# Kernel optimization log

Measured on AMD Instinct MI355X. Metric: run time of the kernel, lower is better.

Reference implementation:

```python
import jax, jax.numpy as jnp
import numpy as np

B, H = 32, 1024  # seq_len == hidden_size (required by the original code's shapes)
S = H

def setup_inputs() -> dict:
    key = jax.random.key(0)
    k1, k2, k3, k4, k5 = jax.random.split(key, 5)
    hidden = jax.random.normal(k1, (B, H), dtype=jnp.float32)
    encoder_outputs = jax.random.normal(k2, (B, S, H), dtype=jnp.float32)
    # nn.Linear(2H -> H): weight [H, 2H], bias [H]
    lim = 1.0 / np.sqrt(2 * H)
    W = jax.random.uniform(k3, (H, 2 * H), dtype=jnp.float32, minval=-lim, maxval=lim)
    b = jax.random.uniform(k4, (H,), dtype=jnp.float32, minval=-lim, maxval=lim)
    # v ~ Normal(0, 1/H)
    v = jax.random.normal(k5, (H,), dtype=jnp.float32) * (1.0 / H)
    return {"hidden": hidden, "encoder_outputs": encoder_outputs, "W": W, "b": b, "v": v}

def reference(hidden, encoder_outputs, W, b, v):
    # hidden: [B, H]; encoder_outputs: [B, S, H] with S == H
    S_len = encoder_outputs.shape[1]
    h_rep = jnp.broadcast_to(hidden[:, None, :], (hidden.shape[0], S_len, hidden.shape[1]))
    enc_t = jnp.swapaxes(encoder_outputs, 1, 2)  # [B, H, S] == [B, S, H] (square)
    x = jnp.concatenate([h_rep, enc_t], axis=2)  # [B, S, 2H]
    energy = jnp.tanh(jnp.einsum('bsk,hk->bsh', x, W) + b)  # [B, S, H]
    # scores[b,s] = sum_h v[h] * energy[b,s,h], softmax over s
    scores = jax.nn.softmax(jnp.einsum('h,bsh->bs', v, energy), axis=1)  # [B, S]
    # bmm(scores[B,1,S], enc_t.transpose(1,2)=encoder_outputs[B,S,H]) -> [B, H]
    context = jnp.einsum('bs,bsh->bh', scores, encoder_outputs)
    return context, scores[:, None, :]
```

## Files before the change

### kernel.cpp

```cpp
#include <hip/hip_runtime.h>
#include <hip/hip_bf16.h>
#include <math.h>

#define B_ 32
#define H_ 1024
#define S_ 1024

typedef __bf16 bf16x4_t __attribute__((ext_vector_type(4)));
typedef __bf16 bf16x8_t __attribute__((ext_vector_type(8)));
typedef float  f32x4_t  __attribute__((ext_vector_type(4)));
typedef float  f32x16_t __attribute__((ext_vector_type(16)));

__device__ __forceinline__ void gl_lds16(const void* g, void* l) {
    __builtin_amdgcn_global_load_lds(
        (const __attribute__((address_space(1))) uint32_t*)g,
        (__attribute__((address_space(3))) uint32_t*)l,
        16, 0, 0);
}

__device__ __forceinline__ float tanh_fast(float x) {
    float e = __builtin_amdgcn_exp2f(x * 2.885390081777927f);
    return 1.f - 2.f * __builtin_amdgcn_rcpf(e + 1.f);
}

__global__ __launch_bounds__(256) void prep_kernel(
    const float* __restrict__ enc, const float* __restrict__ W,
    const float* __restrict__ hidden, const float* __restrict__ bias,
    __bf16* __restrict__ encT, __bf16* __restrict__ W2b,
    float* __restrict__ t1)
{
    __shared__ float T[64 * 65];
    const int idx = blockIdx.x;
    const int tid = threadIdx.x;
    if (idx < 8192) {
        const int b  = idx >> 8;
        const int k0 = ((idx >> 4) & 15) * 64;
        const int s0 = (idx & 15) * 64;
        #pragma unroll
        for (int it = 0; it < 4; ++it) {
            int flat = tid + it * 256;
            int r = flat >> 4, c4 = flat & 15;
            float4 vv = *reinterpret_cast<const float4*>(
                enc + ((size_t)b * S_ + k0 + r) * H_ + s0 + c4 * 4);
            T[r * 65 + c4 * 4 + 0] = vv.x;
            T[r * 65 + c4 * 4 + 1] = vv.y;
            T[r * 65 + c4 * 4 + 2] = vv.z;
            T[r * 65 + c4 * 4 + 3] = vv.w;
        }
        __syncthreads();
        #pragma unroll
        for (int it = 0; it < 2; ++it) {
            int flat = tid + it * 256;
            int s = flat >> 3, ko = flat & 7;
            bf16x8_t p;
            #pragma unroll
            for (int j = 0; j < 8; ++j)
                p[j] = (__bf16)T[(ko * 8 + j) * 65 + s];
            *reinterpret_cast<bf16x8_t*>(
                encT + ((size_t)b * S_ + s0 + s) * H_ + k0 + ko * 8) = p;
        }
    } else if (idx < 9216) {
        int i2 = (idx - 8192) * 1024 + tid * 4;
        int h = i2 >> 10, c = i2 & 1023;
        float4 vv = *reinterpret_cast<const float4*>(W + (size_t)h * (2 * H_) + H_ + c);
        bf16x4_t p = { (__bf16)vv.x, (__bf16)vv.y, (__bf16)vv.z, (__bf16)vv.w };
        *reinterpret_cast<bf16x4_t*>(W2b + (size_t)h * H_ + c) = p;
    } else {
        int h    = (idx - 9216) * 4 + (tid >> 6);
        int lane = tid & 63;
        const float4* wp = reinterpret_cast<const float4*>(W + (size_t)h * (2 * H_));
        float4 w0 = wp[lane], w1 = wp[lane + 64], w2 = wp[lane + 128], w3 = wp[lane + 192];
        float bh = bias[h];
        for (int b = 0; b < B_; ++b) {
            const float4* hp = reinterpret_cast<const float4*>(hidden + b * H_);
            float4 h0 = hp[lane], h1 = hp[lane + 64], h2 = hp[lane + 128], h3 = hp[lane + 192];
            float a = w0.x*h0.x + w0.y*h0.y + w0.z*h0.z + w0.w*h0.w
                    + w1.x*h1.x + w1.y*h1.y + w1.z*h1.z + w1.w*h1.w
                    + w2.x*h2.x + w2.y*h2.y + w2.z*h2.z + w2.w*h2.w
                    + w3.x*h3.x + w3.y*h3.y + w3.z*h3.z + w3.w*h3.w;
            #pragma unroll
            for (int off = 1; off < 64; off <<= 1) a += __shfl_xor(a, off);
            if (lane == 0) t1[b * H_ + h] = a + bh;
        }
    }
}

#define BK2 32

__global__ __launch_bounds__(256) void energy_kernel(
    const __bf16* __restrict__ W2b, const __bf16* __restrict__ encT,
    const float* __restrict__ t1, const float* __restrict__ v,
    float* __restrict__ logits)
{
    __shared__ __align__(16) __bf16 As[2][128 * BK2];
    __shared__ __align__(16) __bf16 Bs[2][128 * BK2];

    const int b     = blockIdx.z;
    const int h0    = blockIdx.x * 128;
    const int s0    = blockIdx.y * 128;
    const int tid   = threadIdx.x;
    const int lane  = tid & 63;
    const int wid   = tid >> 6;
    const int wm    = (wid & 1) * 64;
    const int wn    = (wid >> 1) * 64;
    const int l32   = lane & 31;
    const int khalf = lane >> 5;

    const __bf16* gA[2]; const __bf16* gB[2]; int lofs[2];
    #pragma unroll
    for (int i = 0; i < 2; ++i) {
        int f   = tid + i * 256;
        int row = f >> 2;
        int c   = (f & 3) ^ ((row >> 3) & 3);
        gA[i]   = W2b + (size_t)(h0 + row) * H_ + c * 8;
        gB[i]   = encT + ((size_t)b * S_ + s0 + row) * H_ + c * 8;
        lofs[i] = f * 8;
    }

    #pragma unroll
    for (int i = 0; i < 2; ++i) {
        gl_lds16(gA[i], &As[0][lofs[i]]);
        gl_lds16(gB[i], &Bs[0][lofs[i]]);
    }
    __syncthreads();

    f32x16_t acc[2][2] = {};
    const int pswz = (l32 >> 3) & 3;

    for (int it = 0; it < H_ / BK2; ++it) {
        const int cur = it & 1, nxt = cur ^ 1;
        if (it < H_ / BK2 - 1) {
            const int k1 = (it + 1) * BK2;
            #pragma unroll
            for (int i = 0; i < 2; ++i) {
                gl_lds16(gA[i] + k1, &As[nxt][lofs[i]]);
                gl_lds16(gB[i] + k1, &Bs[nxt][lofs[i]]);
            }
        }
        #pragma unroll
        for (int ks = 0; ks < 2; ++ks) {
            int p8 = ((khalf + 2 * ks) ^ pswz) * 8;
            bf16x8_t a0 = *reinterpret_cast<const bf16x8_t*>(&As[cur][(wm      + l32) * BK2 + p8]);
            bf16x8_t a1 = *reinterpret_cast<const bf16x8_t*>(&As[cur][(wm + 32 + l32) * BK2 + p8]);
            bf16x8_t b0 = *reinterpret_cast<const bf16x8_t*>(&Bs[cur][(wn      + l32) * BK2 + p8]);
            bf16x8_t b1 = *reinterpret_cast<const bf16x8_t*>(&Bs[cur][(wn + 32 + l32) * BK2 + p8]);
            acc[0][0] = __builtin_amdgcn_mfma_f32_32x32x16_bf16(a0, b0, acc[0][0], 0, 0, 0);
            acc[0][1] = __builtin_amdgcn_mfma_f32_32x32x16_bf16(a0, b1, acc[0][1], 0, 0, 0);
            acc[1][0] = __builtin_amdgcn_mfma_f32_32x32x16_bf16(a1, b0, acc[1][0], 0, 0, 0);
            acc[1][1] = __builtin_amdgcn_mfma_f32_32x32x16_bf16(a1, b1, acc[1][1], 0, 0, 0);
        }
        __syncthreads();
    }

    float pn0 = 0.f, pn1 = 0.f;
    #pragma unroll
    for (int mt = 0; mt < 2; ++mt)
        #pragma unroll
        for (int r = 0; r < 16; ++r) {
            int row = wm + mt * 32 + (r & 3) + 8 * (r >> 2) + 4 * khalf;
            int h = h0 + row;
            float tv = t1[b * H_ + h];
            float vv = v[h];
            pn0 += vv * tanh_fast(acc[mt][0][r] + tv);
            pn1 += vv * tanh_fast(acc[mt][1][r] + tv);
        }
    pn0 += __shfl_xor(pn0, 32);
    pn1 += __shfl_xor(pn1, 32);
    if (lane < 32) {
        atomicAdd(&logits[(size_t)b * S_ + s0 + wn + l32], pn0);
        atomicAdd(&logits[(size_t)b * S_ + s0 + wn + 32 + l32], pn1);
    }
}

__global__ __launch_bounds__(256) void ctx_kernel(
    const __bf16* __restrict__ encT, const float* __restrict__ logits,
    float* __restrict__ scores, float* __restrict__ ctx)
{
    __shared__ float sc[1024];
    __shared__ float red[8];
    const int b    = blockIdx.y;
    const int hb   = blockIdx.x * 64;
    const int tid  = threadIdx.x;
    const int lane = tid & 63;
    const int w    = tid >> 6;

    float4 lg = *reinterpret_cast<const float4*>(logits + (size_t)b * S_ + tid * 4);
    float mx = fmaxf(fmaxf(lg.x, lg.y), fmaxf(lg.z, lg.w));
    #pragma unroll
    for (int off = 1; off < 64; off <<= 1) mx = fmaxf(mx, __shfl_xor(mx, off));
    if (lane == 0) red[w] = mx;
    __syncthreads();
    mx = fmaxf(fmaxf(red[0], red[1]), fmaxf(red[2], red[3]));
    const float L2E = 1.44269504088896f;
    float e0 = __builtin_amdgcn_exp2f((lg.x - mx) * L2E);
    float e1 = __builtin_amdgcn_exp2f((lg.y - mx) * L2E);
    float e2 = __builtin_amdgcn_exp2f((lg.z - mx) * L2E);
    float e3 = __builtin_amdgcn_exp2f((lg.w - mx) * L2E);
    float s = e0 + e1 + e2 + e3;
    #pragma unroll
    for (int off = 1; off < 64; off <<= 1) s += __shfl_xor(s, off);
    if (lane == 0) red[4 + w] = s;
    __syncthreads();
    float inv = 1.f / (red[4] + red[5] + red[6] + red[7]);
    float4 sv = { e0 * inv, e1 * inv, e2 * inv, e3 * inv };
    *reinterpret_cast<float4*>(&sc[tid * 4]) = sv;
    if (blockIdx.x == 0)
        *reinterpret_cast<float4*>(scores + (size_t)b * S_ + tid * 4) = sv;
    __syncthreads();

    for (int r = 0; r < 16; ++r) {
        int h = hb + w * 16 + r;
        const __bf16* rp = encT + ((size_t)b * S_ + h) * H_;
        float acc = 0.f;
        #pragma unroll
        for (int c = 0; c < 2; ++c) {
            int s8 = (lane + c * 64) * 8;
            bf16x8_t ev = *reinterpret_cast<const bf16x8_t*>(&rp[s8]);
            float4 sa = *reinterpret_cast<const float4*>(&sc[s8]);
            float4 sb = *reinterpret_cast<const float4*>(&sc[s8 + 4]);
            acc += (float)ev[0]*sa.x + (float)ev[1]*sa.y + (float)ev[2]*sa.z + (float)ev[3]*sa.w
                 + (float)ev[4]*sb.x + (float)ev[5]*sb.y + (float)ev[6]*sb.z + (float)ev[7]*sb.w;
        }
        #pragma unroll
        for (int off = 1; off < 64; off <<= 1) acc += __shfl_xor(acc, off);
        if (lane == 0) ctx[(size_t)b * H_ + h] = acc;
    }
}

extern "C" void kernel_launch(void* const* d_in, const int* in_sizes, int n_in,
                              void* d_out, int out_size, void* d_ws, size_t ws_size,
                              hipStream_t stream)
{
    (void)in_sizes; (void)n_in; (void)out_size; (void)ws_size;
    const float* hidden = (const float*)d_in[0];
    const float* enc    = (const float*)d_in[1];
    const float* W      = (const float*)d_in[2];
    const float* bias   = (const float*)d_in[3];
    const float* v      = (const float*)d_in[4];

    float* out    = (float*)d_out;
    float* ctx    = out;
    float* scores = out + B_ * H_;

    float*  logits = (float*)d_ws;
    float*  t1     = logits + B_ * S_;
    __bf16* W2b    = (__bf16*)(t1 + B_ * H_);
    __bf16* encT   = W2b + (size_t)H_ * H_;

    hipMemsetAsync(logits, 0, (size_t)B_ * S_ * sizeof(float), stream);

    prep_kernel<<<dim3(8192 + 1024 + 256), 256, 0, stream>>>(
        enc, W, hidden, bias, encT, W2b, t1);
    energy_kernel<<<dim3(H_ / 128, S_ / 128, B_), 256, 0, stream>>>(
        W2b, encT, t1, v, logits);
    ctx_kernel<<<dim3(H_ / 64, B_), 256, 0, stream>>>(encT, logits, scores, ctx);
}
```

Baseline: 328.3 us.

## Switch energy GEMM to FP8 MFMA with pre-tiled operand layout

```diff
diff --git a/kernel.cpp b/kernel.cpp
--- a/kernel.cpp
+++ b/kernel.cpp
@@ -6,16 +6,16 @@
 #define H_ 1024
 #define S_ 1024
 
-typedef __bf16 bf16x4_t __attribute__((ext_vector_type(4)));
-typedef __bf16 bf16x8_t __attribute__((ext_vector_type(8)));
 typedef float  f32x4_t  __attribute__((ext_vector_type(4)));
 typedef float  f32x16_t __attribute__((ext_vector_type(16)));
+typedef long long i64;
+typedef i64 i64x2 __attribute__((ext_vector_type(2)));
+typedef unsigned char u8;
 
 __device__ __forceinline__ void gl_lds16(const void* g, void* l) {
     __builtin_amdgcn_global_load_lds(
-        (const __attribute__((address_space(1))) uint32_t*)g,
-        (__attribute__((address_space(3))) uint32_t*)l,
-        16, 0, 0);
+        (const __attribute__((address_space(1))) unsigned int*)g,
+        (__attribute__((address_space(3))) unsigned int*)l, 16, 0, 0);
 }
 
 __device__ __forceinline__ float tanh_fast(float x) {
@@ -23,11 +23,16 @@
     return 1.f - 2.f * __builtin_amdgcn_rcpf(e + 1.f);
 }
 
+__device__ __forceinline__ int kperm(int k) {
+    return (k & ~24) | ((k & 8) << 1) | ((k & 16) >> 1);
+}
+
 __global__ __launch_bounds__(256) void prep_kernel(
     const float* __restrict__ enc, const float* __restrict__ W,
     const float* __restrict__ hidden, const float* __restrict__ bias,
-    __bf16* __restrict__ encT, __bf16* __restrict__ W2b,
-    float* __restrict__ t1)
+    u8* __restrict__ encF8, u8* __restrict__ W2f8,
+    float* __restrict__ t1, float* __restrict__ logits,
+    float* __restrict__ ctx)
 {
     __shared__ float T[64 * 65];
     const int idx = blockIdx.x;
@@ -48,23 +53,44 @@
             T[r * 65 + c4 * 4 + 3] = vv.w;
         }
         __syncthreads();
-        #pragma unroll
-        for (int it = 0; it < 2; ++it) {
-            int flat = tid + it * 256;
-            int s = flat >> 3, ko = flat & 7;
-            bf16x8_t p;
+        {
+            int c   = tid & 1;
+            int ktl = (tid >> 1) & 1;
+            int s   = tid >> 2;
+            int w4[4];
             #pragma unroll
-            for (int j = 0; j < 8; ++j)
-                p[j] = (__bf16)T[(ko * 8 + j) * 65 + s];
-            *reinterpret_cast<bf16x8_t*>(
-                encT + ((size_t)b * S_ + s0 + s) * H_ + k0 + ko * 8) = p;
+            for (int w = 0; w < 4; ++w) {
+                float f[4];
+                #pragma unroll
+                for (int u = 0; u < 4; ++u) {
+                    int i   = w * 4 + u;
+                    int k32 = 16 * (i >> 3) + 8 * c + (i & 7);
+                    f[u] = T[(ktl * 32 + k32) * 65 + s];
+                }
+                int pw = __builtin_amdgcn_cvt_pk_fp8_f32(f[0], f[1], 0, false);
+                pw     = __builtin_amdgcn_cvt_pk_fp8_f32(f[2], f[3], pw, true);
+                w4[w] = pw;
+            }
+            int4 payload = { w4[0], w4[1], w4[2], w4[3] };
+            *reinterpret_cast<int4*>(
+                encF8 + (size_t)b * 1048576 + (size_t)((k0 >> 5) + ktl) * 32768
+                + (size_t)(s0 + s) * 32 + c * 16) = payload;
         }
     } else if (idx < 9216) {
-        int i2 = (idx - 8192) * 1024 + tid * 4;
-        int h = i2 >> 10, c = i2 & 1023;
-        float4 vv = *reinterpret_cast<const float4*>(W + (size_t)h * (2 * H_) + H_ + c);
-        bf16x4_t p = { (__bf16)vv.x, (__bf16)vv.y, (__bf16)vv.z, (__bf16)vv.w };
-        *reinterpret_cast<bf16x4_t*>(W2b + (size_t)h * H_ + c) = p;
+        int h = idx - 8192;
+        if (tid < 64) {
+            int z = h * 64 + tid;
+            if (z < B_ * S_) logits[z] = 0.f;
+            else             ctx[z - B_ * S_] = 0.f;
+        }
+        int kt = tid >> 3;
+        int q  = tid & 7;
+        int src = kperm(q * 4);
+        float4 wv = *reinterpret_cast<const float4*>(
+            W + (size_t)h * (2 * H_) + H_ + kt * 32 + src);
+        int pw = __builtin_amdgcn_cvt_pk_fp8_f32(wv.x * 64.f, wv.y * 64.f, 0, false);
+        pw     = __builtin_amdgcn_cvt_pk_fp8_f32(wv.z * 64.f, wv.w * 64.f, pw, true);
+        *reinterpret_cast<int*>(W2f8 + (size_t)kt * 32768 + (size_t)h * 32 + q * 4) = pw;
     } else {
         int h    = (idx - 9216) * 4 + (tid >> 6);
         int lane = tid & 63;
@@ -85,15 +111,13 @@
     }
 }
 
-#define BK2 32
-
 __global__ __launch_bounds__(256) void energy_kernel(
-    const __bf16* __restrict__ W2b, const __bf16* __restrict__ encT,
+    const u8* __restrict__ W2f8, const u8* __restrict__ encF8,
     const float* __restrict__ t1, const float* __restrict__ v,
     float* __restrict__ logits)
 {
-    __shared__ __align__(16) __bf16 As[2][128 * BK2];
-    __shared__ __align__(16) __bf16 Bs[2][128 * BK2];
+    __shared__ __align__(16) u8 As[2][4096];
+    __shared__ __align__(16) u8 Bs[2][4096];
 
     const int b     = blockIdx.z;
     const int h0    = blockIdx.x * 128;
@@ -106,49 +130,39 @@
     const int l32   = lane & 31;
     const int khalf = lane >> 5;
 
-    const __bf16* gA[2]; const __bf16* gB[2]; int lofs[2];
-    #pragma unroll
-    for (int i = 0; i < 2; ++i) {
-        int f   = tid + i * 256;
-        int row = f >> 2;
-        int c   = (f & 3) ^ ((row >> 3) & 3);
-        gA[i]   = W2b + (size_t)(h0 + row) * H_ + c * 8;
-        gB[i]   = encT + ((size_t)b * S_ + s0 + row) * H_ + c * 8;
-        lofs[i] = f * 8;
-    }
-
-    #pragma unroll
-    for (int i = 0; i < 2; ++i) {
-        gl_lds16(gA[i], &As[0][lofs[i]]);
-        gl_lds16(gB[i], &Bs[0][lofs[i]]);
-    }
+    const int rowl = ((lane & 3) << 3) | ((lane >> 2) & 7);
+    const int row  = (wid << 5) | rowl;
+    const int cch  = lane >> 5;
+    const size_t gofsA = (size_t)(h0 + row) * 32 + cch * 16;
+    const size_t gofsB = (size_t)b * 1048576 + (size_t)(s0 + row) * 32 + cch * 16;
+
+    gl_lds16(W2f8 + gofsA, &As[0][tid * 16]);
+    gl_lds16(encF8 + gofsB, &Bs[0][tid * 16]);
     __syncthreads();
 
     f32x16_t acc[2][2] = {};
-    const int pswz = (l32 >> 3) & 3;
-
-    for (int it = 0; it < H_ / BK2; ++it) {
-        const int cur = it & 1, nxt = cur ^ 1;
-        if (it < H_ / BK2 - 1) {
-            const int k1 = (it + 1) * BK2;
-            #pragma unroll
-            for (int i = 0; i < 2; ++i) {
-                gl_lds16(gA[i] + k1, &As[nxt][lofs[i]]);
-                gl_lds16(gB[i] + k1, &Bs[nxt][lofs[i]]);
-            }
-        }
-        #pragma unroll
-        for (int ks = 0; ks < 2; ++ks) {
-            int p8 = ((khalf + 2 * ks) ^ pswz) * 8;
-            bf16x8_t a0 = *reinterpret_cast<const bf16x8_t*>(&As[cur][(wm      + l32) * BK2 + p8]);
-            bf16x8_t a1 = *reinterpret_cast<const bf16x8_t*>(&As[cur][(wm + 32 + l32) * BK2 + p8]);
-            bf16x8_t b0 = *reinterpret_cast<const bf16x8_t*>(&Bs[cur][(wn      + l32) * BK2 + p8]);
-            bf16x8_t b1 = *reinterpret_cast<const bf16x8_t*>(&Bs[cur][(wn + 32 + l32) * BK2 + p8]);
-            acc[0][0] = __builtin_amdgcn_mfma_f32_32x32x16_bf16(a0, b0, acc[0][0], 0, 0, 0);
-            acc[0][1] = __builtin_amdgcn_mfma_f32_32x32x16_bf16(a0, b1, acc[0][1], 0, 0, 0);
-            acc[1][0] = __builtin_amdgcn_mfma_f32_32x32x16_bf16(a1, b0, acc[1][0], 0, 0, 0);
-            acc[1][1] = __builtin_amdgcn_mfma_f32_32x32x16_bf16(a1, b1, acc[1][1], 0, 0, 0);
-        }
+    const int sl  = ((((l32 & 7) << 2) | (l32 >> 3)) | (khalf << 5)) * 16;
+    const int wAo = (wm >> 5) * 1024;
+    const int wBo = (wn >> 5) * 1024;
+
+    for (int kt = 0; kt < 32; ++kt) {
+        const int cur = kt & 1, nxt = cur ^ 1;
+        if (kt < 31) {
+            gl_lds16(W2f8 + gofsA + (size_t)(kt + 1) * 32768, &As[nxt][tid * 16]);
+            gl_lds16(encF8 + gofsB + (size_t)(kt + 1) * 32768, &Bs[nxt][tid * 16]);
+        }
+        i64x2 a0 = *reinterpret_cast<const i64x2*>(&As[cur][wAo + sl]);
+        i64x2 a1 = *reinterpret_cast<const i64x2*>(&As[cur][wAo + 1024 + sl]);
+        i64x2 b0 = *reinterpret_cast<const i64x2*>(&Bs[cur][wBo + sl]);
+        i64x2 b1 = *reinterpret_cast<const i64x2*>(&Bs[cur][wBo + 1024 + sl]);
+        acc[0][0] = __builtin_amdgcn_mfma_f32_32x32x16_fp8_fp8(a0.x, b0.x, acc[0][0], 0, 0, 0);
+        acc[0][1] = __builtin_amdgcn_mfma_f32_32x32x16_fp8_fp8(a0.x, b1.x, acc[0][1], 0, 0, 0);
+        acc[1][0] = __builtin_amdgcn_mfma_f32_32x32x16_fp8_fp8(a1.x, b0.x, acc[1][0], 0, 0, 0);
+        acc[1][1] = __builtin_amdgcn_mfma_f32_32x32x16_fp8_fp8(a1.x, b1.x, acc[1][1], 0, 0, 0);
+        acc[0][0] = __builtin_amdgcn_mfma_f32_32x32x16_fp8_fp8(a0.y, b0.y, acc[0][0], 0, 0, 0);
+        acc[0][1] = __builtin_amdgcn_mfma_f32_32x32x16_fp8_fp8(a0.y, b1.y, acc[0][1], 0, 0, 0);
+        acc[1][0] = __builtin_amdgcn_mfma_f32_32x32x16_fp8_fp8(a1.y, b0.y, acc[1][0], 0, 0, 0);
+        acc[1][1] = __builtin_amdgcn_mfma_f32_32x32x16_fp8_fp8(a1.y, b1.y, acc[1][1], 0, 0, 0);
         __syncthreads();
     }
 
@@ -157,12 +171,12 @@
     for (int mt = 0; mt < 2; ++mt)
         #pragma unroll
         for (int r = 0; r < 16; ++r) {
-            int row = wm + mt * 32 + (r & 3) + 8 * (r >> 2) + 4 * khalf;
-            int h = h0 + row;
+            int rr = wm + mt * 32 + (r & 3) + 8 * (r >> 2) + 4 * khalf;
+            int h = h0 + rr;
             float tv = t1[b * H_ + h];
             float vv = v[h];
-            pn0 += vv * tanh_fast(acc[mt][0][r] + tv);
-            pn1 += vv * tanh_fast(acc[mt][1][r] + tv);
+            pn0 += vv * tanh_fast(acc[mt][0][r] * 0.015625f + tv);
+            pn1 += vv * tanh_fast(acc[mt][1][r] * 0.015625f + tv);
         }
     pn0 += __shfl_xor(pn0, 32);
     pn1 += __shfl_xor(pn1, 32);
@@ -173,13 +187,13 @@
 }
 
 __global__ __launch_bounds__(256) void ctx_kernel(
-    const __bf16* __restrict__ encT, const float* __restrict__ logits,
+    const float* __restrict__ enc, const float* __restrict__ logits,
     float* __restrict__ scores, float* __restrict__ ctx)
 {
     __shared__ float sc[1024];
     __shared__ float red[8];
     const int b    = blockIdx.y;
-    const int hb   = blockIdx.x * 64;
+    const int s0   = blockIdx.x * 128;
     const int tid  = threadIdx.x;
     const int lane = tid & 63;
     const int w    = tid >> 6;
@@ -208,23 +222,22 @@
         *reinterpret_cast<float4*>(scores + (size_t)b * S_ + tid * 4) = sv;
     __syncthreads();
 
-    for (int r = 0; r < 16; ++r) {
-        int h = hb + w * 16 + r;
-        const __bf16* rp = encT + ((size_t)b * S_ + h) * H_;
-        float acc = 0.f;
-        #pragma unroll
-        for (int c = 0; c < 2; ++c) {
-            int s8 = (lane + c * 64) * 8;
-            bf16x8_t ev = *reinterpret_cast<const bf16x8_t*>(&rp[s8]);
-            float4 sa = *reinterpret_cast<const float4*>(&sc[s8]);
-            float4 sb = *reinterpret_cast<const float4*>(&sc[s8 + 4]);
-            acc += (float)ev[0]*sa.x + (float)ev[1]*sa.y + (float)ev[2]*sa.z + (float)ev[3]*sa.w
-                 + (float)ev[4]*sb.x + (float)ev[5]*sb.y + (float)ev[6]*sb.z + (float)ev[7]*sb.w;
-        }
-        #pragma unroll
-        for (int off = 1; off < 64; off <<= 1) acc += __shfl_xor(acc, off);
-        if (lane == 0) ctx[(size_t)b * H_ + h] = acc;
-    }
+    f32x4_t accv = {0.f, 0.f, 0.f, 0.f};
+    const float* ebase = enc + ((size_t)b * S_ + s0) * H_ + tid * 4;
+    #pragma unroll 4
+    for (int si = 0; si < 128; ++si) {
+        float wgt = sc[s0 + si];
+        float4 ev = *reinterpret_cast<const float4*>(ebase + (size_t)si * H_);
+        accv[0] += wgt * ev.x;
+        accv[1] += wgt * ev.y;
+        accv[2] += wgt * ev.z;
+        accv[3] += wgt * ev.w;
+    }
+    float* cp = ctx + (size_t)b * H_ + tid * 4;
+    atomicAdd(cp + 0, accv[0]);
+    atomicAdd(cp + 1, accv[1]);
+    atomicAdd(cp + 2, accv[2]);
+    atomicAdd(cp + 3, accv[3]);
 }
 
 extern "C" void kernel_launch(void* const* d_in, const int* in_sizes, int n_in,
@@ -242,16 +255,14 @@
     float* ctx    = out;
     float* scores = out + B_ * H_;
 
-    float*  logits = (float*)d_ws;
-    float*  t1     = logits + B_ * S_;
-    __bf16* W2b    = (__bf16*)(t1 + B_ * H_);
-    __bf16* encT   = W2b + (size_t)H_ * H_;
-
-    hipMemsetAsync(logits, 0, (size_t)B_ * S_ * sizeof(float), stream);
+    float* logits = (float*)d_ws;
+    float* t1     = logits + B_ * S_;
+    u8*    W2f8   = (u8*)(t1 + B_ * H_);
+    u8*    encF8  = W2f8 + (size_t)H_ * H_;
 
     prep_kernel<<<dim3(8192 + 1024 + 256), 256, 0, stream>>>(
-        enc, W, hidden, bias, encT, W2b, t1);
+        enc, W, hidden, bias, encF8, W2f8, t1, logits, ctx);
     energy_kernel<<<dim3(H_ / 128, S_ / 128, B_), 256, 0, stream>>>(
-        W2b, encT, t1, v, logits);
-    ctx_kernel<<<dim3(H_ / 64, B_), 256, 0, stream>>>(encT, logits, scores, ctx);
-}
+        W2f8, encF8, t1, v, logits);
+    ctx_kernel<<<dim3(S_ / 128, B_), 256, 0, stream>>>(enc, logits, scores, ctx);
+}
```

New measurement: 312.9 us. -4.7%, faster.
